# Optimization experiments

Measured on AMD Instinct MI355X. Metric: run time of the kernel, lower is better.

Reference implementation:

```python
import jax, jax.numpy as jnp
import numpy as np

D_MODEL = 1024
N_HEADS = 8
D_KEYS = 128
D_LLM = 4096


def setup_inputs() -> dict:
    key = jax.random.key(0)
    ks = jax.random.split(key, 12)
    B, L, S = 8, 1024, 1000
    dk = D_KEYS * N_HEADS  # 1024
    inp = {
        "target_embedding": jax.random.normal(ks[0], (B, L, D_MODEL), jnp.float32),
        "source_embedding": jax.random.normal(ks[1], (S, D_LLM), jnp.float32),
        "value_embedding": jax.random.normal(ks[2], (S, D_LLM), jnp.float32),
        # nn.Linear weights are [out_features, in_features]
        "Wq": jax.random.normal(ks[3], (dk, D_MODEL), jnp.float32) * 0.02,
        "bq": jnp.zeros((dk,), jnp.float32),
        "Wk": jax.random.normal(ks[4], (dk, D_LLM), jnp.float32) * 0.02,
        "bk": jnp.zeros((dk,), jnp.float32),
        "Wv": jax.random.normal(ks[5], (dk, D_LLM), jnp.float32) * 0.02,
        "bv": jnp.zeros((dk,), jnp.float32),
        "Wo": jax.random.normal(ks[6], (D_LLM, dk), jnp.float32) * 0.02,
        "bo": jnp.zeros((D_LLM,), jnp.float32),
    }
    return inp


def reference(target_embedding, source_embedding, value_embedding,
              Wq, bq, Wk, bk, Wv, bv, Wo, bo):
    B, L, _ = target_embedding.shape
    S, _ = source_embedding.shape
    H, E = N_HEADS, D_KEYS
    # projections (torch Linear: x @ W.T + b)
    q = (target_embedding @ Wq.T + bq).reshape(B, L, H, E)
    k = (source_embedding @ Wk.T + bk).reshape(S, H, E)
    v = (value_embedding @ Wv.T + bv).reshape(S, H, E)
    scale = 1.0 / np.sqrt(E).astype(np.float32)
    # cross-attention of B*L queries over S shared prototypes
    scores = jnp.einsum('blhe,she->bhls', q, k)  # [B,H,L,S]
    A = jax.nn.softmax(scale * scores, axis=-1)  # dropout is identity in eval
    out = jnp.einsum('bhls,she->blhe', A, v).reshape(B, L, H * E)
    return out @ Wo.T + bo  # [B, L, D_LLM]
```

## Files before the change

### kernel.cpp

```cpp
#include <hip/hip_runtime.h>
#include <hip/hip_bf16.h>


typedef __attribute__((ext_vector_type(8))) short short8;
typedef __attribute__((ext_vector_type(4))) short short4v;
typedef __attribute__((ext_vector_type(4))) float f32x4;
typedef __attribute__((ext_vector_type(4))) int int4v;

#define DEVINL static __device__ __forceinline__

DEVINL unsigned short f2bf(float f) {
  union { float f; unsigned u; } v; v.f = f;
  unsigned r = v.u + 0x7FFFu + ((v.u >> 16) & 1u);
  return (unsigned short)(r >> 16);
}

DEVINL f32x4 zero4() { f32x4 z; z[0] = 0.f; z[1] = 0.f; z[2] = 0.f; z[3] = 0.f; return z; }
DEVINL short8 zero8() { short8 z; z[0]=0; z[1]=0; z[2]=0; z[3]=0; z[4]=0; z[5]=0; z[6]=0; z[7]=0; return z; }

DEVINL void load_lds16(const unsigned short* g, unsigned short* l) {
  __builtin_amdgcn_global_load_lds(
      (const __attribute__((address_space(1))) void*)g,
      (__attribute__((address_space(3))) void*)l, 16, 0, 0);
}

__global__ __launch_bounds__(256)
void cvt3_bf16(const float* __restrict__ s0, unsigned short* __restrict__ d0, int n0,
               const float* __restrict__ s1, unsigned short* __restrict__ d1, int n1,
               const float* __restrict__ s2, unsigned short* __restrict__ d2, int n2)
{
  int idx = (blockIdx.x * 256 + threadIdx.x) * 8;
  const float* s; unsigned short* d; int rel = idx;
  if (rel < n0) { s = s0; d = d0; }
  else {
    rel -= n0;
    if (rel < n1) { s = s1; d = d1; }
    else { rel -= n1; if (rel >= n2) return; s = s2; d = d2; }
  }
  f32x4 x0 = *(const f32x4*)(s + rel);
  f32x4 x1 = *(const f32x4*)(s + rel + 4);
  short8 o;
#pragma unroll
  for (int j = 0; j < 4; j++) { o[j] = (short)f2bf(x0[j]); o[4 + j] = (short)f2bf(x1[j]); }
  *(short8*)(d + rel) = o;
}

__global__ __launch_bounds__(512, 2)
void gemm256(const unsigned short* __restrict__ A,
             const unsigned short* __restrict__ B,
             const float* __restrict__ bias, float cscale,
             float* __restrict__ C, int M, int N, int K)
{
  __shared__ unsigned short lds[49152];
  const int tid = threadIdx.x;
  const int lane = tid & 63, w = tid >> 6;
  const int wr = w >> 2, wc = w & 3;
  const int l15 = lane & 15, l4 = lane >> 4;

  const int nwg = gridDim.x;
  const int q8 = nwg >> 3;
  const int swz = (blockIdx.x & 7) * q8 + (blockIdx.x >> 3);
  const int nbx = N >> 8;
  const int bx = swz % nbx, by = swz / nbx;
  const int m0 = by << 8, n0 = bx << 8;

  const unsigned short* gA[2];
  const unsigned short* gB[2];
#pragma unroll
  for (int i = 0; i < 2; i++) {
    const int c = i * 512 + tid;
    const int row = 2 * (c >> 3) + ((c >> 2) & 1);
    const int k4 = (c & 3) ^ ((c >> 3) & 3);
    gA[i] = A + (size_t)(m0 + row) * K + k4 * 8;
    gB[i] = B + (size_t)(n0 + row) * K + k4 * 8;
  }

  const int e = wr * 128 + l15;
  const int f = wc * 64 + l15;
  const unsigned cA0 = ((unsigned)(e >> 1) << 7) + ((e & 1) << 6) + ((l4 ^ ((e >> 1) & 3)) << 4);
  const unsigned cB0 = 16384u + ((unsigned)(f >> 1) << 7) + ((f & 1) << 6) + ((l4 ^ ((f >> 1) & 3)) << 4);
  const char* ldsc = (const char*)lds;

  f32x4 acc[8][4];
#pragma unroll
  for (int i = 0; i < 8; i++)
#pragma unroll
    for (int j = 0; j < 4; j++) acc[i][j] = zero4();

  const int NT = K >> 5;

#pragma unroll
  for (int pt = 0; pt < 2; pt++) {
    unsigned short* db = lds + pt * 16384;
#pragma unroll
    for (int i = 0; i < 2; i++) {
      load_lds16(gA[i] + pt * 32, db + (i * 512 + w * 64) * 8);
      load_lds16(gB[i] + pt * 32, db + ((i + 2) * 512 + w * 64) * 8);
    }
  }
  asm volatile("s_waitcnt vmcnt(4)" ::: "memory");
  __builtin_amdgcn_sched_barrier(0);
  __builtin_amdgcn_s_barrier();
  __builtin_amdgcn_sched_barrier(0);

  int bcur = 0, bstg = 2;
  for (int t = 0; t < NT; ++t) {
    if (t + 2 < NT) {
      unsigned short* db = lds + bstg * 16384;
      const int kt = (t + 2) * 32;
#pragma unroll
      for (int i = 0; i < 2; i++) {
        load_lds16(gA[i] + kt, db + (i * 512 + w * 64) * 8);
        load_lds16(gB[i] + kt, db + ((i + 2) * 512 + w * 64) * 8);
      }
    }
    const unsigned bufb = (unsigned)bcur * 32768u;
    const short8* pA = (const short8*)(ldsc + bufb + cA0);
    const short8* pB = (const short8*)(ldsc + bufb + cB0);
    short8 af[8], bfr[4];
#pragma unroll
    for (int mt = 0; mt < 8; mt++) af[mt] = pA[mt * 64];
#pragma unroll
    for (int nt = 0; nt < 4; nt++) bfr[nt] = pB[nt * 64];

    __builtin_amdgcn_s_setprio(1);
#pragma unroll
    for (int mt = 0; mt < 8; mt++)
#pragma unroll
      for (int nt = 0; nt < 4; nt++)
        acc[mt][nt] = __builtin_amdgcn_mfma_f32_16x16x32_bf16(af[mt], bfr[nt], acc[mt][nt], 0, 0, 0);
    __builtin_amdgcn_s_setprio(0);

    if (t + 1 < NT) {
      if (t + 2 < NT) asm volatile("s_waitcnt vmcnt(4)" ::: "memory");
      else            asm volatile("s_waitcnt vmcnt(0)" ::: "memory");
      __builtin_amdgcn_sched_barrier(0);
      __builtin_amdgcn_s_barrier();
      __builtin_amdgcn_sched_barrier(0);
    }
    bcur = (bcur == 2) ? 0 : bcur + 1;
    bstg = (bstg == 2) ? 0 : bstg + 1;
  }

#pragma unroll
  for (int nt = 0; nt < 4; nt++) {
    const int col = n0 + wc * 64 + nt * 16 + l15;
    const float bvv = bias[col];
#pragma unroll
    for (int mt = 0; mt < 8; mt++) {
      const int row = m0 + wr * 128 + mt * 16 + l4 * 4;
#pragma unroll
      for (int j = 0; j < 4; j++)
        C[(size_t)(row + j) * N + col] = (acc[mt][nt][j] + bvv) * cscale;
    }
  }
}

template<bool C_BF16>
__global__ __launch_bounds__(256)
void gemm_bb(const unsigned short* __restrict__ A,
             const unsigned short* __restrict__ B,
             const float* __restrict__ bias, float cscale, void* __restrict__ C_,
             int M, int N, int K)
{
  __shared__ unsigned short As[4096];
  __shared__ unsigned short Bs[4096];
  const int t = threadIdx.x;
  const int lane = t & 63, w = t >> 6;
  const int wm = w >> 1, wn = w & 1;
  const int l15 = lane & 15, l4 = lane >> 4;
  const int m0 = blockIdx.y * 128, n0 = blockIdx.x * 128;

  const int srow = w * 32 + (lane >> 2);
  const int scol = (lane & 3) * 8;
  const unsigned short* Ap = A + (size_t)(m0 + srow) * K + scol;
  const unsigned short* Bp = B + (size_t)(n0 + srow) * K + scol;
  unsigned short* AsW = &As[w * 1024];
  unsigned short* BsW = &Bs[w * 1024];

  f32x4 acc[4][4];
#pragma unroll
  for (int i = 0; i < 4; i++)
#pragma unroll
    for (int j = 0; j < 4; j++) acc[i][j] = zero4();

  for (int k0 = 0; k0 < K; k0 += 32) {
    if (k0) __syncthreads();
    load_lds16(Ap + k0, AsW);
    load_lds16(Ap + k0 + (size_t)16 * K, AsW + 512);
    load_lds16(Bp + k0, BsW);
    load_lds16(Bp + k0 + (size_t)16 * K, BsW + 512);
    __syncthreads();

    short8 af[4], bf[4];
#pragma unroll
    for (int mt = 0; mt < 4; mt++)
      af[mt] = *(const short8*)&As[(wm * 64 + mt * 16 + l15) * 32 + l4 * 8];
#pragma unroll
    for (int nt = 0; nt < 4; nt++)
      bf[nt] = *(const short8*)&Bs[(wn * 64 + nt * 16 + l15) * 32 + l4 * 8];
#pragma unroll
    for (int mt = 0; mt < 4; mt++)
#pragma unroll
      for (int nt = 0; nt < 4; nt++)
        acc[mt][nt] = __builtin_amdgcn_mfma_f32_16x16x32_bf16(af[mt], bf[nt], acc[mt][nt], 0, 0, 0);
  }

#pragma unroll
  for (int nt = 0; nt < 4; nt++) {
    const int col = n0 + wn * 64 + nt * 16 + l15;
    const float bvv = bias[col];
#pragma unroll
    for (int mt = 0; mt < 4; mt++) {
#pragma unroll
      for (int j = 0; j < 4; j++) {
        const int row = m0 + wm * 64 + mt * 16 + l4 * 4 + j;
        const float val = (acc[mt][nt][j] + bvv) * cscale;
        if constexpr (C_BF16)
          ((unsigned short*)C_)[(size_t)row * N + col] = f2bf(val);
        else
          ((float*)C_)[(size_t)row * N + col] = val;
      }
    }
  }
}

template<bool A_BF16, bool C_BF16, bool C_T>
__global__ __launch_bounds__(256)
void gemm_bt(const void* __restrict__ A_, const float* __restrict__ B,
             const float* __restrict__ bias, float cscale, void* __restrict__ C_,
             int M, int N, int K)
{
  __shared__ unsigned short As[128][40];
  __shared__ unsigned short Bs[128][40];
  const int t = threadIdx.x;
  const int lane = t & 63, w = t >> 6;
  const int wm = w >> 1, wn = w & 1;
  const int l15 = lane & 15, l4 = lane >> 4;
  const int m0 = blockIdx.y * 128, n0 = blockIdx.x * 128;
  const int srow = t >> 1, scol = (t & 1) * 16;

  f32x4 acc[4][4];
#pragma unroll
  for (int i = 0; i < 4; i++)
#pragma unroll
    for (int j = 0; j < 4; j++) acc[i][j] = zero4();

  const int am = m0 + srow;
  const int bn = n0 + srow;

  for (int k0 = 0; k0 < K; k0 += 32) {
    short8 av0, av1, bv0, bv1;
    if constexpr (A_BF16) {
      const unsigned short* A = (const unsigned short*)A_;
      if (am < M) {
        const unsigned short* p = A + (size_t)am * K + k0 + scol;
        av0 = *(const short8*)p;
        av1 = *(const short8*)(p + 8);
      } else { av0 = zero8(); av1 = zero8(); }
    } else {
      const float* A = (const float*)A_;
      if (am < M) {
        const float* p = A + (size_t)am * K + k0 + scol;
        f32x4 x0 = *(const f32x4*)(p);
        f32x4 x1 = *(const f32x4*)(p + 4);
        f32x4 x2 = *(const f32x4*)(p + 8);
        f32x4 x3 = *(const f32x4*)(p + 12);
#pragma unroll
        for (int i = 0; i < 4; i++) {
          av0[i]     = (short)f2bf(x0[i]);
          av0[4 + i] = (short)f2bf(x1[i]);
          av1[i]     = (short)f2bf(x2[i]);
          av1[4 + i] = (short)f2bf(x3[i]);
        }
      } else { av0 = zero8(); av1 = zero8(); }
    }
    {
      const float* p = B + (size_t)bn * K + k0 + scol;
      f32x4 x0 = *(const f32x4*)(p);
      f32x4 x1 = *(const f32x4*)(p + 4);
      f32x4 x2 = *(const f32x4*)(p + 8);
      f32x4 x3 = *(const f32x4*)(p + 12);
#pragma unroll
      for (int i = 0; i < 4; i++) {
        bv0[i]     = (short)f2bf(x0[i]);
        bv0[4 + i] = (short)f2bf(x1[i]);
        bv1[i]     = (short)f2bf(x2[i]);
        bv1[4 + i] = (short)f2bf(x3[i]);
      }
    }
    __syncthreads();
    *(short8*)&As[srow][scol]     = av0;
    *(short8*)&As[srow][scol + 8] = av1;
    *(short8*)&Bs[srow][scol]     = bv0;
    *(short8*)&Bs[srow][scol + 8] = bv1;
    __syncthreads();

    short8 af[4], bf[4];
#pragma unroll
    for (int mt = 0; mt < 4; mt++)
      af[mt] = *(const short8*)&As[wm * 64 + mt * 16 + l15][l4 * 8];
#pragma unroll
    for (int nt = 0; nt < 4; nt++)
      bf[nt] = *(const short8*)&Bs[wn * 64 + nt * 16 + l15][l4 * 8];
#pragma unroll
    for (int mt = 0; mt < 4; mt++)
#pragma unroll
      for (int nt = 0; nt < 4; nt++)
        acc[mt][nt] = __builtin_amdgcn_mfma_f32_16x16x32_bf16(af[mt], bf[nt], acc[mt][nt], 0, 0, 0);
  }

#pragma unroll
  for (int nt = 0; nt < 4; nt++) {
    const int col = n0 + wn * 64 + nt * 16 + l15;
    const float bvv = bias[col];
#pragma unroll
    for (int mt = 0; mt < 4; mt++) {
#pragma unroll
      for (int j = 0; j < 4; j++) {
        const int row = m0 + wm * 64 + mt * 16 + l4 * 4 + j;
        if (row < M) {
          float val = (acc[mt][nt][j] + bvv) * cscale;
          if constexpr (C_T)
            ((unsigned short*)C_)[(size_t)col * 1024 + row] = f2bf(val);
          else if constexpr (C_BF16)
            ((unsigned short*)C_)[(size_t)row * N + col] = f2bf(val);
          else
            ((float*)C_)[(size_t)row * N + col] = val;
        }
      }
    }
  }
}

__global__ __launch_bounds__(256)
void gemm_splitk_kv(const float* __restrict__ Src, const float* __restrict__ Val,
                    const float* __restrict__ Wk, const float* __restrict__ Wv,
                    float* __restrict__ Pt, int M, int N, int Ktot)
{
  __shared__ unsigned short As[128][40];
  __shared__ unsigned short Bs[128][40];
  const int t = threadIdx.x;
  const int lane = t & 63, w = t >> 6;
  const int wm = w >> 1, wn = w & 1;
  const int l15 = lane & 15, l4 = lane >> 4;
  const int m0 = blockIdx.y * 128, n0 = blockIdx.x * 128;
  const int srow = t >> 1, scol = (t & 1) * 16;

  const int split = blockIdx.z & 3;
  const int tensor = blockIdx.z >> 2;
  const float* A = tensor ? Val : Src;
  const float* B = tensor ? Wv : Wk;
  const int kchunk = Ktot >> 2;
  const int k_begin = split * kchunk;
  const int k_end = k_begin + kchunk;

  f32x4 acc[4][4];
#pragma unroll
  for (int i = 0; i < 4; i++)
#pragma unroll
    for (int j = 0; j < 4; j++) acc[i][j] = zero4();

  const int am = m0 + srow;
  const int bn = n0 + srow;

  for (int k0 = k_begin; k0 < k_end; k0 += 32) {
    short8 av0, av1, bv0, bv1;
    if (am < M) {
      const float* p = A + (size_t)am * Ktot + k0 + scol;
      f32x4 x0 = *(const f32x4*)(p);
      f32x4 x1 = *(const f32x4*)(p + 4);
      f32x4 x2 = *(const f32x4*)(p + 8);
      f32x4 x3 = *(const f32x4*)(p + 12);
#pragma unroll
      for (int i = 0; i < 4; i++) {
        av0[i]     = (short)f2bf(x0[i]);
        av0[4 + i] = (short)f2bf(x1[i]);
        av1[i]     = (short)f2bf(x2[i]);
        av1[4 + i] = (short)f2bf(x3[i]);
      }
    } else { av0 = zero8(); av1 = zero8(); }
    {
      const float* p = B + (size_t)bn * Ktot + k0 + scol;
      f32x4 x0 = *(const f32x4*)(p);
      f32x4 x1 = *(const f32x4*)(p + 4);
      f32x4 x2 = *(const f32x4*)(p + 8);
      f32x4 x3 = *(const f32x4*)(p + 12);
#pragma unroll
      for (int i = 0; i < 4; i++) {
        bv0[i]     = (short)f2bf(x0[i]);
        bv0[4 + i] = (short)f2bf(x1[i]);
        bv1[i]     = (short)f2bf(x2[i]);
        bv1[4 + i] = (short)f2bf(x3[i]);
      }
    }
    __syncthreads();
    *(short8*)&As[srow][scol]     = av0;
    *(short8*)&As[srow][scol + 8] = av1;
    *(short8*)&Bs[srow][scol]     = bv0;
    *(short8*)&Bs[srow][scol + 8] = bv1;
    __syncthreads();

    short8 af[4], bf[4];
#pragma unroll
    for (int mt = 0; mt < 4; mt++)
      af[mt] = *(const short8*)&As[wm * 64 + mt * 16 + l15][l4 * 8];
#pragma unroll
    for (int nt = 0; nt < 4; nt++)
      bf[nt] = *(const short8*)&Bs[wn * 64 + nt * 16 + l15][l4 * 8];
#pragma unroll
    for (int mt = 0; mt < 4; mt++)
#pragma unroll
      for (int nt = 0; nt < 4; nt++)
        acc[mt][nt] = __builtin_amdgcn_mfma_f32_16x16x32_bf16(af[mt], bf[nt], acc[mt][nt], 0, 0, 0);
  }

  if (tensor == 0) {
    float* C = Pt + (size_t)split * 1024000;
#pragma unroll
    for (int nt = 0; nt < 4; nt++) {
      const int col = n0 + wn * 64 + nt * 16 + l15;
#pragma unroll
      for (int mt = 0; mt < 4; mt++) {
#pragma unroll
        for (int j = 0; j < 4; j++) {
          const int row = m0 + wm * 64 + mt * 16 + l4 * 4 + j;
          if (row < M)
            C[(size_t)row * N + col] = acc[mt][nt][j];
        }
      }
    }
  } else {
    float* C = Pt + 4096000 + (size_t)split * 1048576;
#pragma unroll
    for (int nt = 0; nt < 4; nt++) {
      const int col = n0 + wn * 64 + nt * 16 + l15;
#pragma unroll
      for (int mt = 0; mt < 4; mt++) {
        const int row0 = m0 + wm * 64 + mt * 16 + l4 * 4;
        *(f32x4*)&C[(size_t)col * 1024 + row0] = acc[mt][nt];
      }
    }
  }
}

__global__ __launch_bounds__(256)
void reduce_kv2(const float* __restrict__ Pt, const float* __restrict__ bk,
                const float* __restrict__ bv, unsigned short* __restrict__ Kb,
                unsigned short* __restrict__ Vt)
{
  const int bid = blockIdx.x;
  const int t = threadIdx.x;
  if (bid < 1000) {
    const int v4 = bid * 256 + t;
    const float* base = Pt + (size_t)v4 * 4;
    f32x4 s = *(const f32x4*)(base);
#pragma unroll
    for (int sp = 1; sp < 4; sp++) {
      f32x4 p = *(const f32x4*)(base + (size_t)sp * 1024000);
      s[0] += p[0]; s[1] += p[1]; s[2] += p[2]; s[3] += p[3];
    }
    const int col0 = (v4 * 4) & 1023;
    f32x4 bb = *(const f32x4*)(bk + col0);
    short4v o;
#pragma unroll
    for (int j = 0; j < 4; j++) o[j] = (short)f2bf(s[j] + bb[j]);
    *(short4v*)(Kb + (size_t)v4 * 4) = o;
  } else {
    const int v4 = (bid - 1000) * 256 + t;
    const float* base = Pt + 4096000 + (size_t)v4 * 4;
    f32x4 s = *(const f32x4*)(base);
#pragma unroll
    for (int sp = 1; sp < 4; sp++) {
      f32x4 p = *(const f32x4*)(base + (size_t)sp * 1048576);
      s[0] += p[0]; s[1] += p[1]; s[2] += p[2]; s[3] += p[3];
    }
    const int n = (v4 * 4) >> 10;
    const float bb = bv[n];
    short4v o;
#pragma unroll
    for (int j = 0; j < 4; j++) o[j] = (short)f2bf(s[j] + bb);
    *(short4v*)(Vt + (size_t)v4 * 4) = o;
  }
}

__global__ __launch_bounds__(256, 2)
void attn_fused4(const unsigned short* __restrict__ Q,
                 const unsigned short* __restrict__ Kb,
                 const unsigned short* __restrict__ Vt,
                 unsigned short* __restrict__ Ob)
{
  __shared__ unsigned short Ks[2][32][136];
  __shared__ unsigned short Vs[2][128][40];

  const int t = threadIdx.x;
  const int lane = t & 63, w = t >> 6;
  const int g = lane >> 4, q = lane & 15;
  const int qt = blockIdx.x & 7, bh = blockIdx.x >> 3;
  const int b = bh >> 3, h = bh & 7;
  const int qrow0 = b * 1024 + qt * 128 + w * 32;

  const unsigned short* Kh = Kb + h * 128;
  const unsigned short* Vh = Vt + (size_t)h * 128 * 1024;

  short8 qf[2][4];
#pragma unroll
  for (int qn = 0; qn < 2; qn++) {
    const unsigned short* qp = Q + (size_t)(qrow0 + qn * 16 + q) * 1024 + h * 128;
#pragma unroll
    for (int kk = 0; kk < 4; kk++)
      qf[qn][kk] = *(const short8*)(qp + kk * 32 + g * 8);
  }

  f32x4 o[2][8];
#pragma unroll
  for (int qn = 0; qn < 2; qn++)
#pragma unroll
    for (int et = 0; et < 8; et++) o[qn][et] = zero4();
  float m_s[2] = {-__builtin_inff(), -__builtin_inff()};
  float l_s[2] = {0.f, 0.f};

  const int krow = t >> 3, kcol = (t & 7) * 16;
  const int vrow = t >> 1, vcol = (t & 1) * 16;

  {
    const unsigned short* kp = Kh + (size_t)min(krow, 999) * 1024 + kcol;
    short8 ka0 = *(const short8*)kp, ka1 = *(const short8*)(kp + 8);
    const unsigned short* vp = Vh + (size_t)vrow * 1024 + vcol;
    short8 va0 = *(const short8*)vp, va1 = *(const short8*)(vp + 8);
    *(short8*)&Ks[0][krow][kcol]     = ka0;
    *(short8*)&Ks[0][krow][kcol + 8] = ka1;
    *(short8*)&Vs[0][vrow][vcol]     = va0;
    *(short8*)&Vs[0][vrow][vcol + 8] = va1;
  }
  __syncthreads();

  int cur = 0;
  for (int tile = 0; tile < 32; ++tile) {
    const int s0 = tile * 32;
    const bool last = (s0 == 992);

    const int s0n = last ? 992 : s0 + 32;
    const unsigned short* kp = Kh + (size_t)min(s0n + krow, 999) * 1024 + kcol;
    short8 ka0 = *(const short8*)kp, ka1 = *(const short8*)(kp + 8);
    const unsigned short* vp = Vh + (size_t)vrow * 1024 + s0n + vcol;
    short8 va0 = *(const short8*)vp, va1 = *(const short8*)(vp + 8);

    short8 kf[2][4];
#pragma unroll
    for (int sc = 0; sc < 2; sc++)
#pragma unroll
      for (int kk = 0; kk < 4; kk++)
        kf[sc][kk] = *(const short8*)&Ks[cur][sc * 16 + q][kk * 32 + g * 8];

    f32x4 st[2][2];
    __builtin_amdgcn_s_setprio(1);
#pragma unroll
    for (int qn = 0; qn < 2; qn++)
#pragma unroll
      for (int sc = 0; sc < 2; sc++) {
        st[qn][sc] = zero4();
#pragma unroll
        for (int kk = 0; kk < 4; kk++)
          st[qn][sc] = __builtin_amdgcn_mfma_f32_16x16x32_bf16(kf[sc][kk], qf[qn][kk], st[qn][sc], 0, 0, 0);
      }
    __builtin_amdgcn_s_setprio(0);

    short8 vf[8];
#pragma unroll
    for (int et = 0; et < 8; et++)
      vf[et] = *(const short8*)&Vs[cur][et * 16 + q][g * 8];

#pragma unroll
    for (int qn = 0; qn < 2; qn++) {
      float a[8];
#pragma unroll
      for (int sc = 0; sc < 2; sc++)
#pragma unroll
        for (int j = 0; j < 4; j++) {
          float v = st[qn][sc][j];
          if (last) {
            const int sl = s0 + sc * 16 + 4 * g + j;
            v = (sl < 1000) ? v : -__builtin_inff();
          }
          a[sc * 4 + j] = v;
        }
      float pmax = fmaxf(fmaxf(fmaxf(a[0], a[1]), fmaxf(a[2], a[3])),
                         fmaxf(fmaxf(a[4], a[5]), fmaxf(a[6], a[7])));
      pmax = fmaxf(pmax, __shfl_xor(pmax, 16));
      pmax = fmaxf(pmax, __shfl_xor(pmax, 32));
      if (!__all(pmax - m_s[qn] <= 8.0f)) {
        const float mn = fmaxf(m_s[qn], pmax);
        const float alpha = __expf(m_s[qn] - mn);
        m_s[qn] = mn;
        l_s[qn] *= alpha;
#pragma unroll
        for (int et = 0; et < 8; et++)
#pragma unroll
          for (int j = 0; j < 4; j++) o[qn][et][j] *= alpha;
      }
      float e8[8];
#pragma unroll
      for (int k = 0; k < 8; k++) e8[k] = __expf(a[k] - m_s[qn]);
      float rs = ((e8[0] + e8[1]) + (e8[2] + e8[3])) + ((e8[4] + e8[5]) + (e8[6] + e8[7]));
      rs += __shfl_xor(rs, 16);
      rs += __shfl_xor(rs, 32);
      l_s[qn] += rs;

      int D0, D1, D2, D3;
      asm("v_cvt_pk_bf16_f32 %0, %1, %2" : "=v"(D0) : "v"(e8[0]), "v"(e8[1]));
      asm("v_cvt_pk_bf16_f32 %0, %1, %2" : "=v"(D1) : "v"(e8[2]), "v"(e8[3]));
      asm("v_cvt_pk_bf16_f32 %0, %1, %2" : "=v"(D2) : "v"(e8[4]), "v"(e8[5]));
      asm("v_cvt_pk_bf16_f32 %0, %1, %2" : "=v"(D3) : "v"(e8[6]), "v"(e8[7]));
      const int sA = q + ((g & 1) << 5);
      const int sB = sA + 16;
      const int a0 = __shfl(D0, sA), a1 = __shfl(D1, sA);
      const int a2 = __shfl(D2, sA), a3 = __shfl(D3, sA);
      const int b0 = __shfl(D0, sB), b1 = __shfl(D1, sB);
      const int b2 = __shfl(D2, sB), b3 = __shfl(D3, sB);
      const bool hi = (g >= 2);
      int4v pi;
      pi[0] = hi ? a2 : a0;
      pi[1] = hi ? a3 : a1;
      pi[2] = hi ? b2 : b0;
      pi[3] = hi ? b3 : b1;
      const short8 pf = __builtin_bit_cast(short8, pi);

      __builtin_amdgcn_s_setprio(1);
#pragma unroll
      for (int et = 0; et < 8; et++)
        o[qn][et] = __builtin_amdgcn_mfma_f32_16x16x32_bf16(vf[et], pf, o[qn][et], 0, 0, 0);
      __builtin_amdgcn_s_setprio(0);
    }

    *(short8*)&Ks[cur ^ 1][krow][kcol]     = ka0;
    *(short8*)&Ks[cur ^ 1][krow][kcol + 8] = ka1;
    *(short8*)&Vs[cur ^ 1][vrow][vcol]     = va0;
    *(short8*)&Vs[cur ^ 1][vrow][vcol + 8] = va1;
    __syncthreads();
    cur ^= 1;
  }

#pragma unroll
  for (int qn = 0; qn < 2; qn++) {
    const float inv = 1.0f / l_s[qn];
    unsigned short* op = Ob + (size_t)(qrow0 + qn * 16 + q) * 1024 + h * 128;
#pragma unroll
    for (int et = 0; et < 8; et++) {
      short4v o4;
#pragma unroll
      for (int j = 0; j < 4; j++) o4[j] = (short)f2bf(o[qn][et][j] * inv);
      *(short4v*)(op + et * 16 + 4 * g) = o4;
    }
  }
}

extern "C" void kernel_launch(void* const* d_in, const int* in_sizes, int n_in,
                              void* d_out, int out_size, void* d_ws, size_t ws_size,
                              hipStream_t stream) {
  const float* target = (const float*)d_in[0];
  const float* source = (const float*)d_in[1];
  const float* value  = (const float*)d_in[2];
  const float* Wq = (const float*)d_in[3];
  const float* bq = (const float*)d_in[4];
  const float* Wk = (const float*)d_in[5];
  const float* bk = (const float*)d_in[6];
  const float* Wv = (const float*)d_in[7];
  const float* bv = (const float*)d_in[8];
  const float* Wo = (const float*)d_in[9];
  const float* bo = (const float*)d_in[10];
  float* out = (float*)d_out;

  const float SCALE = 0.08838834764831843f;

  char* ws = (char*)d_ws;
  unsigned short* Qb  = (unsigned short*)(ws);
  unsigned short* Kb  = (unsigned short*)(ws + 16777216);
  unsigned short* Vt  = (unsigned short*)(ws + 18825216);
  unsigned short* Tb  = (unsigned short*)(ws + 20922368);
  unsigned short* Ab  = (unsigned short*)(ws + 20922368);
  unsigned short* Wqb = (unsigned short*)(ws + 37699584);
  unsigned short* Wob = (unsigned short*)(ws + 39796736);
  float* Pt = (float*)d_out;
  const size_t WS_NEED = 48185344;

  dim3 blk(256);
  if (ws_size >= WS_NEED) {
    cvt3_bf16<<<dim3(6656), blk, 0, stream>>>(
        target, Tb, 8192 * 1024, Wq, Wqb, 1024 * 1024, Wo, Wob, 4096 * 1024);
    gemm_splitk_kv<<<dim3(8, 8, 8), blk, 0, stream>>>(
        source, value, Wk, Wv, Pt, 1000, 1024, 4096);
    reduce_kv2<<<dim3(2024), blk, 0, stream>>>(Pt, bk, bv, Kb, Vt);
    gemm_bb<true><<<dim3(8, 64), blk, 0, stream>>>(
        Tb, Wqb, bq, SCALE, (void*)Qb, 8192, 1024, 1024);
    attn_fused4<<<dim3(512), blk, 0, stream>>>(Qb, Kb, Vt, Ab);
    gemm256<<<dim3(512), dim3(512), 0, stream>>>(
        Ab, Wob, bo, 1.0f, out, 8192, 4096, 1024);
  } else {
    gemm_bt<false, true, false><<<dim3(8, 64), blk, 0, stream>>>(
        (const void*)target, Wq, bq, SCALE, (void*)Qb, 8192, 1024, 1024);
    gemm_splitk_kv<<<dim3(8, 8, 8), blk, 0, stream>>>(
        source, value, Wk, Wv, Pt, 1000, 1024, 4096);
    reduce_kv2<<<dim3(2024), blk, 0, stream>>>(Pt, bk, bv, Kb, Vt);
    attn_fused4<<<dim3(512), blk, 0, stream>>>(Qb, Kb, Vt, Ab);
    gemm_bt<true, false, false><<<dim3(32, 64), blk, 0, stream>>>(
        (const void*)Ab, Wo, bo, 1.0f, (void*)out, 8192, 4096, 1024);
  }
}
```

Before: 266.2 us.

## Split GEMM k-step into two ping-pong phases interleaving LDS reads, global stages and MFMA

Restructures the inner GEMM loop so each k-tile runs as two half-phases, each computing four M-subtiles. LDS fragment reads and global-to-LDS staging loads (A in the first phase, B in the second) are interleaved with MFMA blocks and separated by extra workgroup barriers. The aim is to overlap memory traffic with compute in a ping-pong style schedule. It adds four barriers per iteration, which can cost synchronization overhead.

```diff
diff --git a/kernel.cpp b/kernel.cpp
--- a/kernel.cpp
+++ b/kernel.cpp
@@ -105,39 +105,62 @@
 
   int bcur = 0, bstg = 2;
   for (int t = 0; t < NT; ++t) {
-    if (t + 2 < NT) {
-      unsigned short* db = lds + bstg * 16384;
-      const int kt = (t + 2) * 32;
-#pragma unroll
-      for (int i = 0; i < 2; i++) {
-        load_lds16(gA[i] + kt, db + (i * 512 + w * 64) * 8);
-        load_lds16(gB[i] + kt, db + ((i + 2) * 512 + w * 64) * 8);
-      }
-    }
     const unsigned bufb = (unsigned)bcur * 32768u;
     const short8* pA = (const short8*)(ldsc + bufb + cA0);
     const short8* pB = (const short8*)(ldsc + bufb + cB0);
-    short8 af[8], bfr[4];
-#pragma unroll
-    for (int mt = 0; mt < 8; mt++) af[mt] = pA[mt * 64];
+    unsigned short* db = lds + bstg * 16384;
+    const int kt = (t + 2) * 32;
+    const bool do_stage = (t + 2 < NT);
+
+    short8 af0[4], bfr[4];
+#pragma unroll
+    for (int mt = 0; mt < 4; mt++) af0[mt] = pA[mt * 64];
 #pragma unroll
     for (int nt = 0; nt < 4; nt++) bfr[nt] = pB[nt * 64];
-
+    if (do_stage) {
+      load_lds16(gA[0] + kt, db + (0 * 512 + w * 64) * 8);
+      load_lds16(gA[1] + kt, db + (1 * 512 + w * 64) * 8);
+    }
+    __builtin_amdgcn_sched_barrier(0);
+    __builtin_amdgcn_s_barrier();
+    asm volatile("s_waitcnt lgkmcnt(0)" ::: "memory");
+    __builtin_amdgcn_sched_barrier(0);
     __builtin_amdgcn_s_setprio(1);
 #pragma unroll
-    for (int mt = 0; mt < 8; mt++)
+    for (int mt = 0; mt < 4; mt++)
 #pragma unroll
       for (int nt = 0; nt < 4; nt++)
-        acc[mt][nt] = __builtin_amdgcn_mfma_f32_16x16x32_bf16(af[mt], bfr[nt], acc[mt][nt], 0, 0, 0);
+        acc[mt][nt] = __builtin_amdgcn_mfma_f32_16x16x32_bf16(af0[mt], bfr[nt], acc[mt][nt], 0, 0, 0);
     __builtin_amdgcn_s_setprio(0);
-
+    __builtin_amdgcn_sched_barrier(0);
+    __builtin_amdgcn_s_barrier();
+
+    short8 af1[4];
+#pragma unroll
+    for (int mt = 0; mt < 4; mt++) af1[mt] = pA[(mt + 4) * 64];
+    if (do_stage) {
+      load_lds16(gB[0] + kt, db + (2 * 512 + w * 64) * 8);
+      load_lds16(gB[1] + kt, db + (3 * 512 + w * 64) * 8);
+    }
+    __builtin_amdgcn_sched_barrier(0);
     if (t + 1 < NT) {
-      if (t + 2 < NT) asm volatile("s_waitcnt vmcnt(4)" ::: "memory");
-      else            asm volatile("s_waitcnt vmcnt(0)" ::: "memory");
+      if (do_stage) asm volatile("s_waitcnt vmcnt(4)" ::: "memory");
+      else          asm volatile("s_waitcnt vmcnt(0)" ::: "memory");
       __builtin_amdgcn_sched_barrier(0);
-      __builtin_amdgcn_s_barrier();
-      __builtin_amdgcn_sched_barrier(0);
-    }
+    }
+    __builtin_amdgcn_s_barrier();
+    asm volatile("s_waitcnt lgkmcnt(0)" ::: "memory");
+    __builtin_amdgcn_sched_barrier(0);
+    __builtin_amdgcn_s_setprio(1);
+#pragma unroll
+    for (int mt = 0; mt < 4; mt++)
+#pragma unroll
+      for (int nt = 0; nt < 4; nt++)
+        acc[mt + 4][nt] = __builtin_amdgcn_mfma_f32_16x16x32_bf16(af1[mt], bfr[nt], acc[mt + 4][nt], 0, 0, 0);
+    __builtin_amdgcn_s_setprio(0);
+    __builtin_amdgcn_sched_barrier(0);
+    __builtin_amdgcn_s_barrier();
+
     bcur = (bcur == 2) ? 0 : bcur + 1;
     bstg = (bstg == 2) ? 0 : bstg + 1;
   }
```

Result: no change. 267.5 us (+0.5%).

## Software-pipeline attention with QK^T one tile ahead, triple-buffered LDS, exp2 softmax

Applied to the files above, without the earlier changes.

The attention kernel now computes the next tile's QK^T MFMAs while the current tile's softmax and PV MFMAs run. This lets the score matrix work overlap the exp/shuffle work that used to stall the MFMA pipe. K/V staging moves to a three-deep LDS ring that prefetches two tiles ahead, which raises shared memory per block. The log2(e) factor is folded into the Q scale, so exp2f replaces __expf and the rescale threshold is adjusted to match. More live registers (stn plus kf) may pressure occupancy under launch_bounds(256,2).

```diff
diff --git a/kernel.cpp b/kernel.cpp
--- a/kernel.cpp
+++ b/kernel.cpp
@@ -485,13 +485,13 @@
 }
 
 __global__ __launch_bounds__(256, 2)
-void attn_fused4(const unsigned short* __restrict__ Q,
+void attn_fused5(const unsigned short* __restrict__ Q,
                  const unsigned short* __restrict__ Kb,
                  const unsigned short* __restrict__ Vt,
                  unsigned short* __restrict__ Ob)
 {
-  __shared__ unsigned short Ks[2][32][136];
-  __shared__ unsigned short Vs[2][128][40];
+  __shared__ unsigned short Ks[3][32][136];
+  __shared__ unsigned short Vs[3][128][40];
 
   const int t = threadIdx.x;
   const int lane = t & 63, w = t >> 6;
@@ -523,38 +523,27 @@
   const int krow = t >> 3, kcol = (t & 7) * 16;
   const int vrow = t >> 1, vcol = (t & 1) * 16;
 
+#pragma unroll
+  for (int pt = 0; pt < 2; pt++) {
+    const unsigned short* kp = Kh + (size_t)(pt * 32 + krow) * 1024 + kcol;
+    short8 ka0 = *(const short8*)kp, ka1 = *(const short8*)(kp + 8);
+    const unsigned short* vp = Vh + (size_t)vrow * 1024 + pt * 32 + vcol;
+    short8 va0 = *(const short8*)vp, va1 = *(const short8*)(vp + 8);
+    *(short8*)&Ks[pt][krow][kcol]     = ka0;
+    *(short8*)&Ks[pt][krow][kcol + 8] = ka1;
+    *(short8*)&Vs[pt][vrow][vcol]     = va0;
+    *(short8*)&Vs[pt][vrow][vcol + 8] = va1;
+  }
+  __syncthreads();
+
+  f32x4 st[2][2];
   {
-    const unsigned short* kp = Kh + (size_t)min(krow, 999) * 1024 + kcol;
-    short8 ka0 = *(const short8*)kp, ka1 = *(const short8*)(kp + 8);
-    const unsigned short* vp = Vh + (size_t)vrow * 1024 + vcol;
-    short8 va0 = *(const short8*)vp, va1 = *(const short8*)(vp + 8);
-    *(short8*)&Ks[0][krow][kcol]     = ka0;
-    *(short8*)&Ks[0][krow][kcol + 8] = ka1;
-    *(short8*)&Vs[0][vrow][vcol]     = va0;
-    *(short8*)&Vs[0][vrow][vcol + 8] = va1;
-  }
-  __syncthreads();
-
-  int cur = 0;
-  for (int tile = 0; tile < 32; ++tile) {
-    const int s0 = tile * 32;
-    const bool last = (s0 == 992);
-
-    const int s0n = last ? 992 : s0 + 32;
-    const unsigned short* kp = Kh + (size_t)min(s0n + krow, 999) * 1024 + kcol;
-    short8 ka0 = *(const short8*)kp, ka1 = *(const short8*)(kp + 8);
-    const unsigned short* vp = Vh + (size_t)vrow * 1024 + s0n + vcol;
-    short8 va0 = *(const short8*)vp, va1 = *(const short8*)(vp + 8);
-
-    short8 kf[2][4];
+    short8 kf0[2][4];
 #pragma unroll
     for (int sc = 0; sc < 2; sc++)
 #pragma unroll
       for (int kk = 0; kk < 4; kk++)
-        kf[sc][kk] = *(const short8*)&Ks[cur][sc * 16 + q][kk * 32 + g * 8];
-
-    f32x4 st[2][2];
-    __builtin_amdgcn_s_setprio(1);
+        kf0[sc][kk] = *(const short8*)&Ks[0][sc * 16 + q][kk * 32 + g * 8];
 #pragma unroll
     for (int qn = 0; qn < 2; qn++)
 #pragma unroll
@@ -562,15 +551,40 @@
         st[qn][sc] = zero4();
 #pragma unroll
         for (int kk = 0; kk < 4; kk++)
-          st[qn][sc] = __builtin_amdgcn_mfma_f32_16x16x32_bf16(kf[sc][kk], qf[qn][kk], st[qn][sc], 0, 0, 0);
-      }
-    __builtin_amdgcn_s_setprio(0);
-
+          st[qn][sc] = __builtin_amdgcn_mfma_f32_16x16x32_bf16(kf0[sc][kk], qf[qn][kk], st[qn][sc], 0, 0, 0);
+      }
+  }
+
+  int bt = 0;
+  for (int tile = 0; tile < 32; ++tile) {
+    const bool last = (tile == 31);
+    const int bt1 = (bt == 2) ? 0 : bt + 1;
+    const int bt2 = (bt1 == 2) ? 0 : bt1 + 1;
+    const bool do_stage = (tile + 2 < 32);
+
+    short8 ka0, ka1, va0, va1;
+    if (do_stage) {
+      const int s0n = (tile + 2) * 32;
+      const unsigned short* kp = Kh + (size_t)min(s0n + krow, 999) * 1024 + kcol;
+      ka0 = *(const short8*)kp; ka1 = *(const short8*)(kp + 8);
+      const unsigned short* vp = Vh + (size_t)vrow * 1024 + s0n + vcol;
+      va0 = *(const short8*)vp; va1 = *(const short8*)(vp + 8);
+    }
+
+    short8 kf[2][4];
+    if (!last) {
+#pragma unroll
+      for (int sc = 0; sc < 2; sc++)
+#pragma unroll
+        for (int kk = 0; kk < 4; kk++)
+          kf[sc][kk] = *(const short8*)&Ks[bt1][sc * 16 + q][kk * 32 + g * 8];
+    }
     short8 vf[8];
 #pragma unroll
     for (int et = 0; et < 8; et++)
-      vf[et] = *(const short8*)&Vs[cur][et * 16 + q][g * 8];
-
+      vf[et] = *(const short8*)&Vs[bt][et * 16 + q][g * 8];
+
+    short8 pf[2];
 #pragma unroll
     for (int qn = 0; qn < 2; qn++) {
       float a[8];
@@ -580,7 +594,7 @@
         for (int j = 0; j < 4; j++) {
           float v = st[qn][sc][j];
           if (last) {
-            const int sl = s0 + sc * 16 + 4 * g + j;
+            const int sl = 992 + sc * 16 + 4 * g + j;
             v = (sl < 1000) ? v : -__builtin_inff();
           }
           a[sc * 4 + j] = v;
@@ -589,9 +603,9 @@
                          fmaxf(fmaxf(a[4], a[5]), fmaxf(a[6], a[7])));
       pmax = fmaxf(pmax, __shfl_xor(pmax, 16));
       pmax = fmaxf(pmax, __shfl_xor(pmax, 32));
-      if (!__all(pmax - m_s[qn] <= 8.0f)) {
+      if (!__all(pmax - m_s[qn] <= 11.54f)) {
         const float mn = fmaxf(m_s[qn], pmax);
-        const float alpha = __expf(m_s[qn] - mn);
+        const float alpha = exp2f(m_s[qn] - mn);
         m_s[qn] = mn;
         l_s[qn] *= alpha;
 #pragma unroll
@@ -601,7 +615,7 @@
       }
       float e8[8];
 #pragma unroll
-      for (int k = 0; k < 8; k++) e8[k] = __expf(a[k] - m_s[qn]);
+      for (int k = 0; k < 8; k++) e8[k] = exp2f(a[k] - m_s[qn]);
       float rs = ((e8[0] + e8[1]) + (e8[2] + e8[3])) + ((e8[4] + e8[5]) + (e8[6] + e8[7]));
       rs += __shfl_xor(rs, 16);
       rs += __shfl_xor(rs, 32);
@@ -624,21 +638,44 @@
       pi[1] = hi ? a3 : a1;
       pi[2] = hi ? b2 : b0;
       pi[3] = hi ? b3 : b1;
-      const short8 pf = __builtin_bit_cast(short8, pi);
-
-      __builtin_amdgcn_s_setprio(1);
+      pf[qn] = __builtin_bit_cast(short8, pi);
+    }
+
+    f32x4 stn[2][2];
+    __builtin_amdgcn_s_setprio(1);
+    if (!last) {
+#pragma unroll
+      for (int qn = 0; qn < 2; qn++)
+#pragma unroll
+        for (int sc = 0; sc < 2; sc++) {
+          stn[qn][sc] = zero4();
+#pragma unroll
+          for (int kk = 0; kk < 4; kk++)
+            stn[qn][sc] = __builtin_amdgcn_mfma_f32_16x16x32_bf16(kf[sc][kk], qf[qn][kk], stn[qn][sc], 0, 0, 0);
+        }
+    }
+#pragma unroll
+    for (int qn = 0; qn < 2; qn++)
 #pragma unroll
       for (int et = 0; et < 8; et++)
-        o[qn][et] = __builtin_amdgcn_mfma_f32_16x16x32_bf16(vf[et], pf, o[qn][et], 0, 0, 0);
-      __builtin_amdgcn_s_setprio(0);
-    }
-
-    *(short8*)&Ks[cur ^ 1][krow][kcol]     = ka0;
-    *(short8*)&Ks[cur ^ 1][krow][kcol + 8] = ka1;
-    *(short8*)&Vs[cur ^ 1][vrow][vcol]     = va0;
-    *(short8*)&Vs[cur ^ 1][vrow][vcol + 8] = va1;
+        o[qn][et] = __builtin_amdgcn_mfma_f32_16x16x32_bf16(vf[et], pf[qn], o[qn][et], 0, 0, 0);
+    __builtin_amdgcn_s_setprio(0);
+
+    if (do_stage) {
+      *(short8*)&Ks[bt2][krow][kcol]     = ka0;
+      *(short8*)&Ks[bt2][krow][kcol + 8] = ka1;
+      *(short8*)&Vs[bt2][vrow][vcol]     = va0;
+      *(short8*)&Vs[bt2][vrow][vcol + 8] = va1;
+    }
     __syncthreads();
-    cur ^= 1;
+    if (!last) {
+#pragma unroll
+      for (int qn = 0; qn < 2; qn++)
+#pragma unroll
+        for (int sc = 0; sc < 2; sc++)
+          st[qn][sc] = stn[qn][sc];
+    }
+    bt = bt1;
   }
 
 #pragma unroll
@@ -671,7 +708,7 @@
   const float* bo = (const float*)d_in[10];
   float* out = (float*)d_out;
 
-  const float SCALE = 0.08838834764831843f;
+  const float SCALE = 0.12751743f;
 
   char* ws = (char*)d_ws;
   unsigned short* Qb  = (unsigned short*)(ws);
@@ -693,7 +730,7 @@
     reduce_kv2<<<dim3(2024), blk, 0, stream>>>(Pt, bk, bv, Kb, Vt);
     gemm_bb<true><<<dim3(8, 64), blk, 0, stream>>>(
         Tb, Wqb, bq, SCALE, (void*)Qb, 8192, 1024, 1024);
-    attn_fused4<<<dim3(512), blk, 0, stream>>>(Qb, Kb, Vt, Ab);
+    attn_fused5<<<dim3(512), blk, 0, stream>>>(Qb, Kb, Vt, Ab);
     gemm256<<<dim3(512), dim3(512), 0, stream>>>(
         Ab, Wob, bo, 1.0f, out, 8192, 4096, 1024);
   } else {
@@ -702,7 +739,7 @@
     gemm_splitk_kv<<<dim3(8, 8, 8), blk, 0, stream>>>(
         source, value, Wk, Wv, Pt, 1000, 1024, 4096);
     reduce_kv2<<<dim3(2024), blk, 0, stream>>>(Pt, bk, bv, Kb, Vt);
-    attn_fused4<<<dim3(512), blk, 0, stream>>>(Qb, Kb, Vt, Ab);
+    attn_fused5<<<dim3(512), blk, 0, stream>>>(Qb, Kb, Vt, Ab);
     gemm_bt<true, false, false><<<dim3(32, 64), blk, 0, stream>>>(
         (const void*)Ab, Wo, bo, 1.0f, (void*)out, 8192, 4096, 1024);
   }
```

Measured after the change: 270.5 us. Within noise of the previous version (+1.6%).

## Pre-convert K/V inputs to bf16 and use direct-to-LDS split-K GEMM

Applied to the files above, without the earlier changes.

Adds a cvt_kv kernel that converts source, value, Wk and Wv to bf16, zero-padding the 1000 source rows to 1024. A new split-K GEMM then streams them with global_load_lds straight into LDS instead of loading fp32 and converting in registers, and drops the row bound checks. Separately, the softmax switches from __expf to exp2f by folding log2(e) into the Q scale and widening the rescale threshold to match. The cost is one extra conversion pass with its memory traffic, plus bf16 staging buffers placed in the output region.

```diff
diff --git a/kernel.cpp b/kernel.cpp
--- a/kernel.cpp
+++ b/kernel.cpp
@@ -43,6 +43,33 @@
 #pragma unroll
   for (int j = 0; j < 4; j++) { o[j] = (short)f2bf(x0[j]); o[4 + j] = (short)f2bf(x1[j]); }
   *(short8*)(d + rel) = o;
+}
+
+__global__ __launch_bounds__(256)
+void cvt_kv(const float* __restrict__ src, const float* __restrict__ val,
+            const float* __restrict__ wk, const float* __restrict__ wv,
+            unsigned short* __restrict__ Sb, unsigned short* __restrict__ Vb,
+            unsigned short* __restrict__ Wkb, unsigned short* __restrict__ Wvb)
+{
+  const int seg = blockIdx.x >> 11;
+  const int e = (((blockIdx.x & 2047) * 256) + threadIdx.x) * 8;
+  const float* s;
+  unsigned short* d;
+  bool pad = false;
+  if (seg == 0)      { s = src; d = Sb;  pad = (e >> 12) >= 1000; }
+  else if (seg == 1) { s = val; d = Vb;  pad = (e >> 12) >= 1000; }
+  else if (seg == 2) { s = wk;  d = Wkb; }
+  else               { s = wv;  d = Wvb; }
+  short8 o;
+  if (pad) {
+    o = zero8();
+  } else {
+    f32x4 x0 = *(const f32x4*)(s + e);
+    f32x4 x1 = *(const f32x4*)(s + e + 4);
+#pragma unroll
+    for (int j = 0; j < 4; j++) { o[j] = (short)f2bf(x0[j]); o[4 + j] = (short)f2bf(x1[j]); }
+  }
+  *(short8*)(d + e) = o;
 }
 
 __global__ __launch_bounds__(512, 2)
@@ -222,6 +249,129 @@
           ((float*)C_)[(size_t)row * N + col] = val;
       }
     }
+  }
+}
+
+__global__ __launch_bounds__(256)
+void gemm_splitk_bb(const unsigned short* __restrict__ Sb,
+                    const unsigned short* __restrict__ Vb,
+                    const unsigned short* __restrict__ Wkb,
+                    const unsigned short* __restrict__ Wvb,
+                    float* __restrict__ Pt)
+{
+  __shared__ unsigned short As[4096];
+  __shared__ unsigned short Bs[4096];
+  const int t = threadIdx.x;
+  const int lane = t & 63, w = t >> 6;
+  const int wm = w >> 1, wn = w & 1;
+  const int l15 = lane & 15, l4 = lane >> 4;
+  const int m0 = blockIdx.y * 128, n0 = blockIdx.x * 128;
+  const int split = blockIdx.z & 3;
+  const int tensor = blockIdx.z >> 2;
+  const unsigned short* A = tensor ? Vb : Sb;
+  const unsigned short* B = tensor ? Wvb : Wkb;
+  const int kb = split * 1024;
+
+  const int srow = w * 32 + (lane >> 2);
+  const int scol = (lane & 3) * 8;
+  const unsigned short* Ap = A + (size_t)(m0 + srow) * 4096 + kb + scol;
+  const unsigned short* Bp = B + (size_t)(n0 + srow) * 4096 + kb + scol;
+  unsigned short* AsW = &As[w * 1024];
+  unsigned short* BsW = &Bs[w * 1024];
+
+  f32x4 acc[4][4];
+#pragma unroll
+  for (int i = 0; i < 4; i++)
+#pragma unroll
+    for (int j = 0; j < 4; j++) acc[i][j] = zero4();
+
+  for (int k0 = 0; k0 < 1024; k0 += 32) {
+    if (k0) __syncthreads();
+    load_lds16(Ap + k0, AsW);
+    load_lds16(Ap + k0 + (size_t)16 * 4096, AsW + 512);
+    load_lds16(Bp + k0, BsW);
+    load_lds16(Bp + k0 + (size_t)16 * 4096, BsW + 512);
+    __syncthreads();
+
+    short8 af[4], bf[4];
+#pragma unroll
+    for (int mt = 0; mt < 4; mt++)
+      af[mt] = *(const short8*)&As[(wm * 64 + mt * 16 + l15) * 32 + l4 * 8];
+#pragma unroll
+    for (int nt = 0; nt < 4; nt++)
+      bf[nt] = *(const short8*)&Bs[(wn * 64 + nt * 16 + l15) * 32 + l4 * 8];
+#pragma unroll
+    for (int mt = 0; mt < 4; mt++)
+#pragma unroll
+      for (int nt = 0; nt < 4; nt++)
+        acc[mt][nt] = __builtin_amdgcn_mfma_f32_16x16x32_bf16(af[mt], bf[nt], acc[mt][nt], 0, 0, 0);
+  }
+
+  if (tensor == 0) {
+    float* C = Pt + (size_t)split * 1048576;
+#pragma unroll
+    for (int nt = 0; nt < 4; nt++) {
+      const int col = n0 + wn * 64 + nt * 16 + l15;
+#pragma unroll
+      for (int mt = 0; mt < 4; mt++) {
+#pragma unroll
+        for (int j = 0; j < 4; j++) {
+          const int row = m0 + wm * 64 + mt * 16 + l4 * 4 + j;
+          C[(size_t)row * 1024 + col] = acc[mt][nt][j];
+        }
+      }
+    }
+  } else {
+    float* C = Pt + 4194304 + (size_t)split * 1048576;
+#pragma unroll
+    for (int nt = 0; nt < 4; nt++) {
+      const int col = n0 + wn * 64 + nt * 16 + l15;
+#pragma unroll
+      for (int mt = 0; mt < 4; mt++) {
+        const int row0 = m0 + wm * 64 + mt * 16 + l4 * 4;
+        *(f32x4*)&C[(size_t)col * 1024 + row0] = acc[mt][nt];
+      }
+    }
+  }
+}
+
+__global__ __launch_bounds__(256)
+void reduce_kv2(const float* __restrict__ Pt, const float* __restrict__ bk,
+                const float* __restrict__ bv, unsigned short* __restrict__ Kb,
+                unsigned short* __restrict__ Vt)
+{
+  const int bid = blockIdx.x;
+  const int t = threadIdx.x;
+  if (bid < 1000) {
+    const int v4 = bid * 256 + t;
+    const float* base = Pt + (size_t)v4 * 4;
+    f32x4 s = *(const f32x4*)(base);
+#pragma unroll
+    for (int sp = 1; sp < 4; sp++) {
+      f32x4 p = *(const f32x4*)(base + (size_t)sp * 1048576);
+      s[0] += p[0]; s[1] += p[1]; s[2] += p[2]; s[3] += p[3];
+    }
+    const int col0 = (v4 * 4) & 1023;
+    f32x4 bb = *(const f32x4*)(bk + col0);
+    short4v o;
+#pragma unroll
+    for (int j = 0; j < 4; j++) o[j] = (short)f2bf(s[j] + bb[j]);
+    *(short4v*)(Kb + (size_t)v4 * 4) = o;
+  } else {
+    const int v4 = (bid - 1000) * 256 + t;
+    const float* base = Pt + 4194304 + (size_t)v4 * 4;
+    f32x4 s = *(const f32x4*)(base);
+#pragma unroll
+    for (int sp = 1; sp < 4; sp++) {
+      f32x4 p = *(const f32x4*)(base + (size_t)sp * 1048576);
+      s[0] += p[0]; s[1] += p[1]; s[2] += p[2]; s[3] += p[3];
+    }
+    const int n = (v4 * 4) >> 10;
+    const float bb = bv[n];
+    short4v o;
+#pragma unroll
+    for (int j = 0; j < 4; j++) o[j] = (short)f2bf(s[j] + bb);
+    *(short4v*)(Vt + (size_t)v4 * 4) = o;
   }
 }
 
@@ -333,157 +483,6 @@
   }
 }
 
-__global__ __launch_bounds__(256)
-void gemm_splitk_kv(const float* __restrict__ Src, const float* __restrict__ Val,
-                    const float* __restrict__ Wk, const float* __restrict__ Wv,
-                    float* __restrict__ Pt, int M, int N, int Ktot)
-{
-  __shared__ unsigned short As[128][40];
-  __shared__ unsigned short Bs[128][40];
-  const int t = threadIdx.x;
-  const int lane = t & 63, w = t >> 6;
-  const int wm = w >> 1, wn = w & 1;
-  const int l15 = lane & 15, l4 = lane >> 4;
-  const int m0 = blockIdx.y * 128, n0 = blockIdx.x * 128;
-  const int srow = t >> 1, scol = (t & 1) * 16;
-
-  const int split = blockIdx.z & 3;
-  const int tensor = blockIdx.z >> 2;
-  const float* A = tensor ? Val : Src;
-  const float* B = tensor ? Wv : Wk;
-  const int kchunk = Ktot >> 2;
-  const int k_begin = split * kchunk;
-  const int k_end = k_begin + kchunk;
-
-  f32x4 acc[4][4];
-#pragma unroll
-  for (int i = 0; i < 4; i++)
-#pragma unroll
-    for (int j = 0; j < 4; j++) acc[i][j] = zero4();
-
-  const int am = m0 + srow;
-  const int bn = n0 + srow;
-
-  for (int k0 = k_begin; k0 < k_end; k0 += 32) {
-    short8 av0, av1, bv0, bv1;
-    if (am < M) {
-      const float* p = A + (size_t)am * Ktot + k0 + scol;
-      f32x4 x0 = *(const f32x4*)(p);
-      f32x4 x1 = *(const f32x4*)(p + 4);
-      f32x4 x2 = *(const f32x4*)(p + 8);
-      f32x4 x3 = *(const f32x4*)(p + 12);
-#pragma unroll
-      for (int i = 0; i < 4; i++) {
-        av0[i]     = (short)f2bf(x0[i]);
-        av0[4 + i] = (short)f2bf(x1[i]);
-        av1[i]     = (short)f2bf(x2[i]);
-        av1[4 + i] = (short)f2bf(x3[i]);
-      }
-    } else { av0 = zero8(); av1 = zero8(); }
-    {
-      const float* p = B + (size_t)bn * Ktot + k0 + scol;
-      f32x4 x0 = *(const f32x4*)(p);
-      f32x4 x1 = *(const f32x4*)(p + 4);
-      f32x4 x2 = *(const f32x4*)(p + 8);
-      f32x4 x3 = *(const f32x4*)(p + 12);
-#pragma unroll
-      for (int i = 0; i < 4; i++) {
-        bv0[i]     = (short)f2bf(x0[i]);
-        bv0[4 + i] = (short)f2bf(x1[i]);
-        bv1[i]     = (short)f2bf(x2[i]);
-        bv1[4 + i] = (short)f2bf(x3[i]);
-      }
-    }
-    __syncthreads();
-    *(short8*)&As[srow][scol]     = av0;
-    *(short8*)&As[srow][scol + 8] = av1;
-    *(short8*)&Bs[srow][scol]     = bv0;
-    *(short8*)&Bs[srow][scol + 8] = bv1;
-    __syncthreads();
-
-    short8 af[4], bf[4];
-#pragma unroll
-    for (int mt = 0; mt < 4; mt++)
-      af[mt] = *(const short8*)&As[wm * 64 + mt * 16 + l15][l4 * 8];
-#pragma unroll
-    for (int nt = 0; nt < 4; nt++)
-      bf[nt] = *(const short8*)&Bs[wn * 64 + nt * 16 + l15][l4 * 8];
-#pragma unroll
-    for (int mt = 0; mt < 4; mt++)
-#pragma unroll
-      for (int nt = 0; nt < 4; nt++)
-        acc[mt][nt] = __builtin_amdgcn_mfma_f32_16x16x32_bf16(af[mt], bf[nt], acc[mt][nt], 0, 0, 0);
-  }
-
-  if (tensor == 0) {
-    float* C = Pt + (size_t)split * 1024000;
-#pragma unroll
-    for (int nt = 0; nt < 4; nt++) {
-      const int col = n0 + wn * 64 + nt * 16 + l15;
-#pragma unroll
-      for (int mt = 0; mt < 4; mt++) {
-#pragma unroll
-        for (int j = 0; j < 4; j++) {
-          const int row = m0 + wm * 64 + mt * 16 + l4 * 4 + j;
-          if (row < M)
-            C[(size_t)row * N + col] = acc[mt][nt][j];
-        }
-      }
-    }
-  } else {
-    float* C = Pt + 4096000 + (size_t)split * 1048576;
-#pragma unroll
-    for (int nt = 0; nt < 4; nt++) {
-      const int col = n0 + wn * 64 + nt * 16 + l15;
-#pragma unroll
-      for (int mt = 0; mt < 4; mt++) {
-        const int row0 = m0 + wm * 64 + mt * 16 + l4 * 4;
-        *(f32x4*)&C[(size_t)col * 1024 + row0] = acc[mt][nt];
-      }
-    }
-  }
-}
-
-__global__ __launch_bounds__(256)
-void reduce_kv2(const float* __restrict__ Pt, const float* __restrict__ bk,
-                const float* __restrict__ bv, unsigned short* __restrict__ Kb,
-                unsigned short* __restrict__ Vt)
-{
-  const int bid = blockIdx.x;
-  const int t = threadIdx.x;
-  if (bid < 1000) {
-    const int v4 = bid * 256 + t;
-    const float* base = Pt + (size_t)v4 * 4;
-    f32x4 s = *(const f32x4*)(base);
-#pragma unroll
-    for (int sp = 1; sp < 4; sp++) {
-      f32x4 p = *(const f32x4*)(base + (size_t)sp * 1024000);
-      s[0] += p[0]; s[1] += p[1]; s[2] += p[2]; s[3] += p[3];
-    }
-    const int col0 = (v4 * 4) & 1023;
-    f32x4 bb = *(const f32x4*)(bk + col0);
-    short4v o;
-#pragma unroll
-    for (int j = 0; j < 4; j++) o[j] = (short)f2bf(s[j] + bb[j]);
-    *(short4v*)(Kb + (size_t)v4 * 4) = o;
-  } else {
-    const int v4 = (bid - 1000) * 256 + t;
-    const float* base = Pt + 4096000 + (size_t)v4 * 4;
-    f32x4 s = *(const f32x4*)(base);
-#pragma unroll
-    for (int sp = 1; sp < 4; sp++) {
-      f32x4 p = *(const f32x4*)(base + (size_t)sp * 1048576);
-      s[0] += p[0]; s[1] += p[1]; s[2] += p[2]; s[3] += p[3];
-    }
-    const int n = (v4 * 4) >> 10;
-    const float bb = bv[n];
-    short4v o;
-#pragma unroll
-    for (int j = 0; j < 4; j++) o[j] = (short)f2bf(s[j] + bb);
-    *(short4v*)(Vt + (size_t)v4 * 4) = o;
-  }
-}
-
 __global__ __launch_bounds__(256, 2)
 void attn_fused4(const unsigned short* __restrict__ Q,
                  const unsigned short* __restrict__ Kb,
@@ -589,9 +588,9 @@
                          fmaxf(fmaxf(a[4], a[5]), fmaxf(a[6], a[7])));
       pmax = fmaxf(pmax, __shfl_xor(pmax, 16));
       pmax = fmaxf(pmax, __shfl_xor(pmax, 32));
-      if (!__all(pmax - m_s[qn] <= 8.0f)) {
+      if (!__all(pmax - m_s[qn] <= 11.54f)) {
         const float mn = fmaxf(m_s[qn], pmax);
-        const float alpha = __expf(m_s[qn] - mn);
+        const float alpha = exp2f(m_s[qn] - mn);
         m_s[qn] = mn;
         l_s[qn] *= alpha;
 #pragma unroll
@@ -601,7 +600,7 @@
       }
       float e8[8];
 #pragma unroll
-      for (int k = 0; k < 8; k++) e8[k] = __expf(a[k] - m_s[qn]);
+      for (int k = 0; k < 8; k++) e8[k] = exp2f(a[k] - m_s[qn]);
       float rs = ((e8[0] + e8[1]) + (e8[2] + e8[3])) + ((e8[4] + e8[5]) + (e8[6] + e8[7]));
       rs += __shfl_xor(rs, 16);
       rs += __shfl_xor(rs, 32);
@@ -671,9 +670,11 @@
   const float* bo = (const float*)d_in[10];
   float* out = (float*)d_out;
 
-  const float SCALE = 0.08838834764831843f;
+  const float SCALE = 0.12751743f;
 
   char* ws = (char*)d_ws;
+  unsigned short* Sb  = (unsigned short*)(ws);
+  unsigned short* Vb  = (unsigned short*)(ws + 8388608);
   unsigned short* Qb  = (unsigned short*)(ws);
   unsigned short* Kb  = (unsigned short*)(ws + 16777216);
   unsigned short* Vt  = (unsigned short*)(ws + 18825216);
@@ -682,14 +683,17 @@
   unsigned short* Wqb = (unsigned short*)(ws + 37699584);
   unsigned short* Wob = (unsigned short*)(ws + 39796736);
   float* Pt = (float*)d_out;
+  unsigned short* Wkb = (unsigned short*)((char*)d_out + 33554432);
+  unsigned short* Wvb = (unsigned short*)((char*)d_out + 41943040);
   const size_t WS_NEED = 48185344;
 
   dim3 blk(256);
   if (ws_size >= WS_NEED) {
     cvt3_bf16<<<dim3(6656), blk, 0, stream>>>(
         target, Tb, 8192 * 1024, Wq, Wqb, 1024 * 1024, Wo, Wob, 4096 * 1024);
-    gemm_splitk_kv<<<dim3(8, 8, 8), blk, 0, stream>>>(
-        source, value, Wk, Wv, Pt, 1000, 1024, 4096);
+    cvt_kv<<<dim3(8192), blk, 0, stream>>>(
+        source, value, Wk, Wv, Sb, Vb, Wkb, Wvb);
+    gemm_splitk_bb<<<dim3(8, 8, 8), blk, 0, stream>>>(Sb, Vb, Wkb, Wvb, Pt);
     reduce_kv2<<<dim3(2024), blk, 0, stream>>>(Pt, bk, bv, Kb, Vt);
     gemm_bb<true><<<dim3(8, 64), blk, 0, stream>>>(
         Tb, Wqb, bq, SCALE, (void*)Qb, 8192, 1024, 1024);
@@ -699,9 +703,10 @@
   } else {
     gemm_bt<false, true, false><<<dim3(8, 64), blk, 0, stream>>>(
         (const void*)target, Wq, bq, SCALE, (void*)Qb, 8192, 1024, 1024);
-    gemm_splitk_kv<<<dim3(8, 8, 8), blk, 0, stream>>>(
-        source, value, Wk, Wv, Pt, 1000, 1024, 4096);
-    reduce_kv2<<<dim3(2024), blk, 0, stream>>>(Pt, bk, bv, Kb, Vt);
+    gemm_bt<false, true, false><<<dim3(8, 8), blk, 0, stream>>>(
+        (const void*)source, Wk, bk, 1.0f, (void*)Kb, 1000, 1024, 4096);
+    gemm_bt<false, true, true><<<dim3(8, 8), blk, 0, stream>>>(
+        (const void*)value, Wv, bv, 1.0f, (void*)Vt, 1000, 1024, 4096);
     attn_fused4<<<dim3(512), blk, 0, stream>>>(Qb, Kb, Vt, Ab);
     gemm_bt<true, false, false><<<dim3(32, 64), blk, 0, stream>>>(
         (const void*)Ab, Wo, bo, 1.0f, (void*)out, 8192, 4096, 1024);
```

After: 251.1 us. -5.7%, faster.
